# Performance work log

Measured on AMD Instinct MI355X. Metric: run time of the kernel, lower is better.

Reference implementation:

```python
import jax, jax.numpy as jnp
import numpy as np

EMBED_DIMS = [8, 16, 8]      # prod = 1024 = embed_dim
HIDDEN_DIMS = [16, 16, 16]   # prod = 4096 = hidden_dim
RANK = 16
B, S = 4, 1024


def _make_cores(key, in_dims, out_dims, rank):
    d = len(in_dims)
    ranks = [1] + [rank] * (d - 1) + [1]
    cores = []
    for k in range(d):
        key, sub = jax.random.split(key)
        shape = (ranks[k], in_dims[k], out_dims[k], ranks[k + 1])
        scale = 1.0 / np.sqrt(in_dims[k] * ranks[k])
        cores.append((scale * jax.random.normal(sub, shape, dtype=jnp.float32)))
    return cores


def setup_inputs() -> dict:
    key = jax.random.key(0)
    k_x, k1, k2, kb1, kb2 = jax.random.split(key, 5)
    x = jax.random.normal(k_x, (B, S, 1024), dtype=jnp.float32)
    fc1 = _make_cores(k1, EMBED_DIMS, HIDDEN_DIMS, RANK)
    fc2 = _make_cores(k2, HIDDEN_DIMS, EMBED_DIMS, RANK)
    b1 = 0.01 * jax.random.normal(kb1, (4096,), dtype=jnp.float32)
    b2 = 0.01 * jax.random.normal(kb2, (1024,), dtype=jnp.float32)
    return {
        "x": x,
        "fc1_c0": fc1[0], "fc1_c1": fc1[1], "fc1_c2": fc1[2], "fc1_b": b1,
        "fc2_c0": fc2[0], "fc2_c1": fc2[1], "fc2_c2": fc2[2], "fc2_b": b2,
    }


def tt_linear(x_flat, cores, bias, in_dims):
    """TT-matrix x batch-of-vectors product. x_flat: [N, prod(in_dims)].

    Cores: core_k has shape [r_{k-1}, n_k, m_k, r_k] with r_0 = r_d = 1.
    Invariant: acc is [r_{k-1}, n_k, rest] with rest laid out as
    (n_{k+1}..n_d, N, m_1..m_{k-1}).
    """
    N = x_flat.shape[0]
    acc = x_flat.reshape((N,) + tuple(in_dims))      # [N, n1..nd]
    acc = jnp.moveaxis(acc, 0, -1)                   # [n1..nd, N]
    acc = acc.reshape(in_dims[0], -1)[None]          # [1, n1, rest]
    d = len(cores)
    for k, c in enumerate(cores):
        # contract previous rank + current input mode
        acc = jnp.einsum('pnR,pnmq->Rmq', acc, c)    # [rest, m_k, r_k]
        if k < d - 1:
            n_next = in_dims[k + 1]
            R, m, q = acc.shape
            acc = acc.reshape(n_next, R // n_next, m, q)
            acc = jnp.transpose(acc, (3, 0, 1, 2)).reshape(q, n_next, -1)
    # final acc: [N * m1..m_{d-1}, m_d, 1] -> [N, M]
    return acc.reshape(N, -1) + bias


def reference(x, fc1_c0, fc1_c1, fc1_c2, fc1_b, fc2_c0, fc2_c1, fc2_c2, fc2_b):
    flat = x.reshape(-1, x.shape[-1])                        # [N, embed_dim]
    z1 = tt_linear(flat, [fc1_c0, fc1_c1, fc1_c2], fc1_b, EMBED_DIMS)   # [N, hidden]
    h1 = jax.nn.gelu(z1, approximate=False)                  # exact erf GELU (torch default)
    z2 = tt_linear(h1, [fc2_c0, fc2_c1, fc2_c2], fc2_b, HIDDEN_DIMS)    # [N, embed]
    return z2.reshape(*x.shape[:-1], z2.shape[-1])
```

## Files before the change

### kernel.cpp

```cpp
#include <hip/hip_runtime.h>
#include <stdint.h>

__device__ __forceinline__ float b2f(unsigned short u) {
    union { uint32_t i; float f; } v; v.i = ((uint32_t)u) << 16; return v.f;
}
__device__ __forceinline__ unsigned short f2b(float f) {
    union { float f; uint32_t i; } v; v.f = f;
    uint32_t r = v.i + 0x7fffu + ((v.i >> 16) & 1u);
    return (unsigned short)(r >> 16);
}

typedef __bf16 bf16x8 __attribute__((ext_vector_type(8)));
typedef float  f32x16 __attribute__((ext_vector_type(16)));

template<int N1, int N2, int N3, int M1, int M2, int M3>
__device__ __forceinline__ void build_W_fused(int blk,
                                              const float* __restrict__ c0,
                                              const float* __restrict__ c1,
                                              const float* __restrict__ c2,
                                              unsigned short* __restrict__ W,
                                              float* __restrict__ S) {
    constexpr int K = N1 * N2 * N3;
    const int n2 = blk / M2;
    const int m2 = blk % M2;

    for (int e = threadIdx.x; e < 16 * N3 * M3; e += 256) {
        const int m3 = e % M3;
        const int n3 = (e / M3) % N3;
        const int r1 = e / (M3 * N3);
        const float* c1p = c1 + ((r1 * N2 + n2) * M2 + m2) * 16;
        float s = 0.f;
#pragma unroll
        for (int r2 = 0; r2 < 16; ++r2)
            s += c1p[r2] * c2[(r2 * N3 + n3) * M3 + m3];
        S[e] = s;
    }
    __syncthreads();

    for (int e = threadIdx.x; e < N1 * M1 * M3; e += 256) {
        const int m3 = e % M3;
        const int m1 = (e / M3) % M1;
        const int n1 = e / (M3 * M1);
        const float* c0p = c0 + (n1 * M1 + m1) * 16;
        float acc[N3] = {};
#pragma unroll
        for (int r1 = 0; r1 < 16; ++r1) {
            const float c0v = c0p[r1];
#pragma unroll
            for (int n3 = 0; n3 < N3; ++n3)
                acc[n3] += c0v * S[(r1 * N3 + n3) * M3 + m3];
        }
        unsigned short ob[N3];
#pragma unroll
        for (int n3 = 0; n3 < N3; ++n3) ob[n3] = f2b(acc[n3]);
        unsigned short* dst = W + (size_t)((m1 * M2 + m2) * M3 + m3) * K
                                + (n1 * N2 + n2) * N3;
#pragma unroll
        for (int c = 0; c < N3 / 8; ++c)
            ((int4*)dst)[c] = ((const int4*)ob)[c];
    }
}

__global__ __launch_bounds__(256)
void prep_all(const float* __restrict__ c10, const float* __restrict__ c11,
              const float* __restrict__ c12,
              const float* __restrict__ c20, const float* __restrict__ c21,
              const float* __restrict__ c22,
              const float* __restrict__ x, unsigned short* __restrict__ xb,
              unsigned short* __restrict__ W1, unsigned short* __restrict__ W2) {
    __shared__ float S[16 * 128];
    const int b = blockIdx.x;
    if (b < 256) {
        build_W_fused<8, 16, 8, 16, 16, 16>(b, c10, c11, c12, W1, S);
    } else if (b < 512) {
        build_W_fused<16, 16, 16, 8, 16, 8>(b - 256, c20, c21, c22, W2, S);
    } else {
        const int t = (b - 512) * 256 + threadIdx.x;
        const float4* p = (const float4*)(x + (size_t)t * 8);
        float4 f0 = p[0], f1 = p[1];
        int4 o;
        o.x = (uint32_t)f2b(f0.x) | ((uint32_t)f2b(f0.y) << 16);
        o.y = (uint32_t)f2b(f0.z) | ((uint32_t)f2b(f0.w) << 16);
        o.z = (uint32_t)f2b(f1.x) | ((uint32_t)f2b(f1.y) << 16);
        o.w = (uint32_t)f2b(f1.z) | ((uint32_t)f2b(f1.w) << 16);
        ((int4*)xb)[t] = o;
    }
}

template<int N3, int M3>
__device__ __forceinline__ void build_T_body(int e,
                                             const float* __restrict__ c1,
                                             const float* __restrict__ c2,
                                             float* __restrict__ T) {
    int m3 = e % M3;
    int t  = e / M3;
    int n3 = t % N3;
    int rm = t / N3;
    float s = 0.f;
#pragma unroll
    for (int r2 = 0; r2 < 16; ++r2)
        s += c1[rm * 16 + r2] * c2[(r2 * N3 + n3) * M3 + m3];
    T[e] = s;
}

__global__ __launch_bounds__(256)
void prep_stage1(const float* __restrict__ c11, const float* __restrict__ c12,
                 float* __restrict__ T1,
                 const float* __restrict__ c21, const float* __restrict__ c22,
                 float* __restrict__ T2,
                 const float* __restrict__ x, unsigned short* __restrict__ xb) {
    const int b = blockIdx.x;
    if (b < 2048) {
        build_T_body<8, 16>(b * 256 + threadIdx.x, c11, c12, T1);
    } else if (b < 4096) {
        build_T_body<16, 8>((b - 2048) * 256 + threadIdx.x, c21, c22, T2);
    } else {
        const int t = (b - 4096) * 256 + threadIdx.x;
        const float4* p = (const float4*)(x + (size_t)t * 8);
        float4 f0 = p[0], f1 = p[1];
        int4 o;
        o.x = (uint32_t)f2b(f0.x) | ((uint32_t)f2b(f0.y) << 16);
        o.y = (uint32_t)f2b(f0.z) | ((uint32_t)f2b(f0.w) << 16);
        o.z = (uint32_t)f2b(f1.x) | ((uint32_t)f2b(f1.y) << 16);
        o.w = (uint32_t)f2b(f1.z) | ((uint32_t)f2b(f1.w) << 16);
        ((int4*)xb)[t] = o;
    }
}

template<int N1, int N2, int N3, int M1, int M2, int M3>
__device__ __forceinline__ void build_W_body(int t,
                                             const float* __restrict__ c0,
                                             const float* __restrict__ T,
                                             unsigned short* __restrict__ W) {
    constexpr int K = N1 * N2 * N3;
    int m3 = t % M3;
    int m2 = (t / M3) % M2;
    int n2 = (t / (M3 * M2)) % N2;
    int m1 = (t / (M3 * M2 * N2)) % M1;
    int n1 =  t / (M3 * M2 * N2 * M1);

    float c0r[16];
    const float4* c0p = (const float4*)(c0 + (n1 * M1 + m1) * 16);
#pragma unroll
    for (int i = 0; i < 4; ++i) ((float4*)c0r)[i] = c0p[i];

    float acc[N3] = {};
#pragma unroll
    for (int r1 = 0; r1 < 16; ++r1) {
        const float* Tp = T + (size_t)(((r1 * 16 + n2) * 16 + m2) * N3) * M3 + m3;
#pragma unroll
        for (int n3 = 0; n3 < N3; ++n3)
            acc[n3] += c0r[r1] * Tp[n3 * M3];
    }

    unsigned short ob[N3];
#pragma unroll
    for (int n3 = 0; n3 < N3; ++n3) ob[n3] = f2b(acc[n3]);

    unsigned short* dst = W + (size_t)((m1 * M2 + m2) * M3 + m3) * K
                            + (n1 * N2 + n2) * N3;
#pragma unroll
    for (int c = 0; c < N3 / 8; ++c)
        ((int4*)dst)[c] = ((const int4*)ob)[c];
}

template<int N1, int N2, int N3, int M1, int M2, int M3>
__global__ __launch_bounds__(256)
void build_W(const float* __restrict__ c0, const float* __restrict__ T,
             unsigned short* __restrict__ W) {
    build_W_body<N1, N2, N3, M1, M2, M3>(blockIdx.x * 256 + threadIdx.x, c0, T, W);
}

template<int BM, int BN, int KTOT, int GX, bool DO_GELU>
__global__ __launch_bounds__(512, 2)
void gemm_big(const unsigned short* __restrict__ A,
              const unsigned short* __restrict__ Bt,
              const float* __restrict__ bias,
              unsigned short* __restrict__ C,
              int Ncols)
{
    constexpr int BK   = 64;
    constexpr int NT   = KTOT / BK;
    constexpr int ASZ  = BM * BK;
    constexpr int BUFE = (BM + BN) * BK;
    constexpr int ACH  = BM / 64;
    constexpr int BCH  = BN / 64;
    constexpr int FI   = 4, FJ = 2;

    extern __shared__ unsigned short sh[];

    const int tid   = threadIdx.x;
    const int lane  = tid & 63;
    const int wave  = tid >> 6;
    const int m32   = lane & 31;
    const int khalf = lane >> 5;
    const int waveM = (wave >> 2) * 128;
    const int waveN = (wave & 3) * 64;
    const int srow  = tid >> 3;
    const int sslot = tid & 7;

    int lin = (int)blockIdx.y * GX + (int)blockIdx.x;
    const int total = GX * (int)gridDim.y;
    lin = (lin & 7) * (total >> 3) + (lin >> 3);
    const int colBase = (lin % GX) * BN;
    const int rowBase = (lin / GX) * BM;

#define BG_STAGE(B_, K0_)                                                     \
    {                                                                         \
        _Pragma("unroll")                                                     \
        for (int c = 0; c < ACH; ++c) {                                       \
            const int r  = c * 64 + srow;                                     \
            const int jg = sslot ^ (r & 7) ^ ((r >> 3) & 7);                  \
            const unsigned short* src = A +                                   \
                (size_t)(rowBase + r) * KTOT + (K0_) + jg * 8;                \
            unsigned short* dst = sh + (B_) * BUFE + c * 4096 + wave * 512;   \
            __builtin_amdgcn_global_load_lds(                                 \
                (const __attribute__((address_space(1))) void*)src,           \
                (__attribute__((address_space(3))) void*)dst, 16, 0, 0);      \
        }                                                                     \
        _Pragma("unroll")                                                     \
        for (int c = 0; c < BCH; ++c) {                                       \
            const int r  = c * 64 + srow;                                     \
            const int jg = sslot ^ (r & 7) ^ ((r >> 3) & 7);                  \
            const unsigned short* src = Bt +                                  \
                (size_t)(colBase + r) * KTOT + (K0_) + jg * 8;                \
            unsigned short* dst = sh + (B_) * BUFE + ASZ + c * 4096           \
                                  + wave * 512;                               \
            __builtin_amdgcn_global_load_lds(                                 \
                (const __attribute__((address_space(1))) void*)src,           \
                (__attribute__((address_space(3))) void*)dst, 16, 0, 0);      \
        }                                                                     \
    }

    f32x16 acc[FI][FJ] = {};

    BG_STAGE(0, 0)
    __syncthreads();

    int buf = 0;
    for (int t = 0; t < NT; ++t) {
        if (t + 1 < NT) BG_STAGE(buf ^ 1, (t + 1) * BK)

        const unsigned short* Ab = sh + buf * BUFE;
        const unsigned short* Bb = Ab + ASZ;
#pragma unroll
        for (int ks = 0; ks < 4; ++ks) {
            bf16x8 a_f[FI], b_f[FJ];
            const int g = ks * 2 + khalf;
#pragma unroll
            for (int i = 0; i < FI; ++i) {
                const int r = waveM + i * 32 + m32;
                const int key = (r & 7) ^ ((r >> 3) & 7);
                a_f[i] = *(const bf16x8*)&Ab[r * BK + ((g ^ key) << 3)];
            }
#pragma unroll
            for (int j = 0; j < FJ; ++j) {
                const int r = waveN + j * 32 + m32;
                const int key = (r & 7) ^ ((r >> 3) & 7);
                b_f[j] = *(const bf16x8*)&Bb[r * BK + ((g ^ key) << 3)];
            }
#pragma unroll
            for (int i = 0; i < FI; ++i)
#pragma unroll
                for (int j = 0; j < FJ; ++j)
                    acc[i][j] = __builtin_amdgcn_mfma_f32_32x32x16_bf16(
                        a_f[i], b_f[j], acc[i][j], 0, 0, 0);
        }
        __syncthreads();
        buf ^= 1;
    }
#undef BG_STAGE

#pragma unroll
    for (int i = 0; i < FI; ++i) {
#pragma unroll
        for (int j = 0; j < FJ; ++j) {
            const int col = colBase + waveN + j * 32 + m32;
            const float bv = bias[col];
#pragma unroll
            for (int reg = 0; reg < 16; ++reg) {
                const int row = rowBase + waveM + i * 32 +
                                (reg & 3) + 8 * (reg >> 2) + 4 * khalf;
                float z = acc[i][j][reg] + bv;
                if (DO_GELU)
                    z = 0.5f * z * (1.f + erff(z * 0.70710678118654752f));
                C[(size_t)row * Ncols + col] = f2b(z);
            }
        }
    }
}

template<int BM, int BN, int KCH, int KSTR, int GX, int GY,
         bool DO_GELU, bool ATOMIC>
__global__ __launch_bounds__(256, 4)
void gemm_sb(const unsigned short* __restrict__ A,
             const unsigned short* __restrict__ Bt,
             const float* __restrict__ bias,
             void* __restrict__ Cv,
             int Ncols)
{
    constexpr int BK  = 64;
    constexpr int NT  = KCH / BK;
    constexpr int ASZ = BM * BK;
    constexpr int ACH = BM / 32;
    constexpr int BCH = BN / 32;
    constexpr int FI  = BM / 64, FJ = BN / 64;

    extern __shared__ unsigned short sh[];

    const int tid   = threadIdx.x;
    const int lane  = tid & 63;
    const int wave  = tid >> 6;
    const int m32   = lane & 31;
    const int khalf = lane >> 5;
    const int waveM = (wave >> 1) * (BM / 2);
    const int waveN = (wave & 1) * (BN / 2);
    const int srow  = tid >> 3;
    const int sslot = tid & 7;

    int lin = ((int)blockIdx.z * GY + (int)blockIdx.y) * GX + (int)blockIdx.x;
    const int total = GX * GY * (int)gridDim.z;
    lin = (lin & 7) * (total >> 3) + (lin >> 3);
    const int colBase = (lin % GX) * BN;
    const int rowBase = ((lin / GX) % GY) * BM;
    const int kOff    = (lin / (GX * GY)) * KCH;

#define SB_STAGE(K0_)                                                         \
    {                                                                         \
        _Pragma("unroll")                                                     \
        for (int c = 0; c < ACH; ++c) {                                       \
            const int r  = c * 32 + srow;                                     \
            const int jg = sslot ^ (r & 7) ^ ((r >> 3) & 7);                  \
            const unsigned short* src = A +                                   \
                (size_t)(rowBase + r) * KSTR + (K0_) + jg * 8;                \
            unsigned short* dst = sh + c * 2048 + wave * 512;                 \
            __builtin_amdgcn_global_load_lds(                                 \
                (const __attribute__((address_space(1))) void*)src,           \
                (__attribute__((address_space(3))) void*)dst, 16, 0, 0);      \
        }                                                                     \
        _Pragma("unroll")                                                     \
        for (int c = 0; c < BCH; ++c) {                                       \
            const int r  = c * 32 + srow;                                     \
            const int jg = sslot ^ (r & 7) ^ ((r >> 3) & 7);                  \
            const unsigned short* src = Bt +                                  \
                (size_t)(colBase + r) * KSTR + (K0_) + jg * 8;                \
            unsigned short* dst = sh + ASZ + c * 2048 + wave * 512;           \
            __builtin_amdgcn_global_load_lds(                                 \
                (const __attribute__((address_space(1))) void*)src,           \
                (__attribute__((address_space(3))) void*)dst, 16, 0, 0);      \
        }                                                                     \
    }

    f32x16 acc[FI][FJ] = {};

    for (int t = 0; t < NT; ++t) {
        SB_STAGE(kOff + t * BK)
        __syncthreads();

        const unsigned short* Ab = sh;
        const unsigned short* Bb = sh + ASZ;
#pragma unroll
        for (int ks = 0; ks < 4; ++ks) {
            bf16x8 a_f[FI], b_f[FJ];
            const int g = ks * 2 + khalf;
#pragma unroll
            for (int i = 0; i < FI; ++i) {
                const int r = waveM + i * 32 + m32;
                const int key = (r & 7) ^ ((r >> 3) & 7);
                a_f[i] = *(const bf16x8*)&Ab[r * BK + ((g ^ key) << 3)];
            }
#pragma unroll
            for (int j = 0; j < FJ; ++j) {
                const int r = waveN + j * 32 + m32;
                const int key = (r & 7) ^ ((r >> 3) & 7);
                b_f[j] = *(const bf16x8*)&Bb[r * BK + ((g ^ key) << 3)];
            }
#pragma unroll
            for (int i = 0; i < FI; ++i)
#pragma unroll
                for (int j = 0; j < FJ; ++j)
                    acc[i][j] = __builtin_amdgcn_mfma_f32_32x32x16_bf16(
                        a_f[i], b_f[j], acc[i][j], 0, 0, 0);
        }
        if (t + 1 < NT) __syncthreads();
    }
#undef SB_STAGE

#pragma unroll
    for (int i = 0; i < FI; ++i) {
#pragma unroll
        for (int j = 0; j < FJ; ++j) {
            const int col = colBase + waveN + j * 32 + m32;
            const float bv = ATOMIC ? 0.f : bias[col];
#pragma unroll
            for (int reg = 0; reg < 16; ++reg) {
                const int row = rowBase + waveM + i * 32 +
                                (reg & 3) + 8 * (reg >> 2) + 4 * khalf;
                const size_t off = (size_t)row * Ncols + col;
                if (ATOMIC) {
                    unsafeAtomicAdd((float*)Cv + off, acc[i][j][reg]);
                } else {
                    float z = acc[i][j][reg] + bv;
                    if (DO_GELU) {
                        z = 0.5f * z * (1.f + erff(z * 0.70710678118654752f));
                        ((unsigned short*)Cv)[off] = f2b(z);
                    } else {
                        ((float*)Cv)[off] = z;
                    }
                }
            }
        }
    }
}

#define PC_COMPUTE(BUF)                                                       \
    {                                                                         \
        _Pragma("unroll")                                                     \
        for (int ks = 0; ks < 4; ++ks) {                                      \
            bf16x8 a_f[FI], b_f[FJ];                                          \
            _Pragma("unroll")                                                 \
            for (int i = 0; i < FI; ++i) {                                    \
                const int key = (m32 & 7) ^                                   \
                    (((waveM >> 3) + 4 * i + (m32 >> 3)) & 7);                \
                const int slot = ((ks * 2 + khalf) ^ key) * 8;                \
                a_f[i] = *(const bf16x8*)&As[(BUF) * ASZ +                    \
                          (waveM + i * 32 + m32) * BK + slot];                \
            }                                                                 \
            _Pragma("unroll")                                                 \
            for (int j = 0; j < FJ; ++j) {                                    \
                const int key = (m32 & 7) ^                                   \
                    (((waveN >> 3) + 4 * j + (m32 >> 3)) & 7);                \
                const int slot = ((ks * 2 + khalf) ^ key) * 8;                \
                b_f[j] = *(const bf16x8*)&Bs[(BUF) * BSZ +                    \
                          (waveN + j * 32 + m32) * BK + slot];                \
            }                                                                 \
            _Pragma("unroll")                                                 \
            for (int i = 0; i < FI; ++i)                                      \
                _Pragma("unroll")                                             \
                for (int j = 0; j < FJ; ++j)                                  \
                    acc[i][j] = __builtin_amdgcn_mfma_f32_32x32x16_bf16(      \
                        a_f[i], b_f[j], acc[i][j], 0, 0, 0);                  \
        }                                                                     \
    }

template<int BM, int BN, int KTOT, bool DO_GELU, bool A_F32, bool C_F32>
__global__ __launch_bounds__(512, 4)
void gemm_pc(const void* __restrict__ Av,
             const unsigned short* __restrict__ Bt,
             const float* __restrict__ bias,
             void* __restrict__ Cv,
             int Ncols) {
    constexpr int BK  = 64;
    constexpr int CA  = BM / 8;
    constexpr int CB  = BN / 8;
    constexpr int PA  = CA / 4;
    constexpr int PB  = CB / 4;
    constexpr int FI  = BM / 64;
    constexpr int FJ  = BN / 64;
    constexpr int ASZ = BM * BK;
    constexpr int BSZ = BN * BK;
    __shared__ unsigned short As[2 * ASZ];
    __shared__ unsigned short Bs[2 * BSZ];

    const int tid  = threadIdx.x;
    const int lane = tid & 63;
    const int wave = tid >> 6;
    const int rowBase = blockIdx.y * BM;
    const int colBase = blockIdx.x * BN;

    const int lr    = lane >> 3;
    const int jj    = lane & 7;
    const int m32   = lane & 31;
    const int khalf = lane >> 5;

    if (wave >= 4) {
        const int pw = wave - 4;
#pragma unroll
        for (int it = 0; it < PA; ++it) {
            const int c  = pw * PA + it;
            const int jg = jj ^ lr ^ (c & 7);
            const size_t aoff = (size_t)(rowBase + c * 8 + lr) * KTOT + jg * 8;
            int4 v;
            if (A_F32) {
                const float* ga = (const float*)Av + aoff;
                float4 f0 = *(const float4*)ga;
                float4 f1 = *(const float4*)(ga + 4);
                v.x = (uint32_t)f2b(f0.x) | ((uint32_t)f2b(f0.y) << 16);
                v.y = (uint32_t)f2b(f0.z) | ((uint32_t)f2b(f0.w) << 16);
                v.z = (uint32_t)f2b(f1.x) | ((uint32_t)f2b(f1.y) << 16);
                v.w = (uint32_t)f2b(f1.z) | ((uint32_t)f2b(f1.w) << 16);
            } else {
                v = *(const int4*)((const unsigned short*)Av + aoff);
            }
            *(int4*)&As[c * 512 + lane * 8] = v;
        }
#pragma unroll
        for (int it = 0; it < PB; ++it) {
            const int c  = pw * PB + it;
            const int jg = jj ^ lr ^ (c & 7);
            *(int4*)&Bs[c * 512 + lane * 8] =
                *(const int4*)(Bt + (size_t)(colBase + c * 8 + lr) * KTOT + jg * 8);
        }
        __syncthreads();

        int buf = 1;
        for (int k0 = BK; k0 < KTOT; k0 += BK) {
            int4 aR[PA], bR[PB];
#pragma unroll
            for (int it = 0; it < PA; ++it) {
                const int c  = pw * PA + it;
                const int jg = jj ^ lr ^ (c & 7);
                const size_t aoff = (size_t)(rowBase + c * 8 + lr) * KTOT + k0 + jg * 8;
                if (A_F32) {
                    const float* ga = (const float*)Av + aoff;
                    float4 f0 = *(const float4*)ga;
                    float4 f1 = *(const float4*)(ga + 4);
                    int4 v;
                    v.x = (uint32_t)f2b(f0.x) | ((uint32_t)f2b(f0.y) << 16);
                    v.y = (uint32_t)f2b(f0.z) | ((uint32_t)f2b(f0.w) << 16);
                    v.z = (uint32_t)f2b(f1.x) | ((uint32_t)f2b(f1.y) << 16);
                    v.w = (uint32_t)f2b(f1.z) | ((uint32_t)f2b(f1.w) << 16);
                    aR[it] = v;
                } else {
                    aR[it] = *(const int4*)((const unsigned short*)Av + aoff);
                }
            }
#pragma unroll
            for (int it = 0; it < PB; ++it) {
                const int c  = pw * PB + it;
                const int jg = jj ^ lr ^ (c & 7);
                bR[it] = *(const int4*)(Bt + (size_t)(colBase + c * 8 + lr) * KTOT + k0 + jg * 8);
            }
#pragma unroll
            for (int it = 0; it < PA; ++it) {
                const int c = pw * PA + it;
                *(int4*)&As[buf * ASZ + c * 512 + lane * 8] = aR[it];
            }
#pragma unroll
            for (int it = 0; it < PB; ++it) {
                const int c = pw * PB + it;
                *(int4*)&Bs[buf * BSZ + c * 512 + lane * 8] = bR[it];
            }
            __syncthreads();
            buf ^= 1;
        }
    } else {
        const int waveM = (wave >> 1) * (BM / 2);
        const int waveN = (wave & 1) * (BN / 2);
        f32x16 acc[FI][FJ] = {};

        __syncthreads();

        int cur = 0;
        for (int k0 = BK; k0 < KTOT; k0 += BK) {
            PC_COMPUTE(cur)
            __syncthreads();
            cur ^= 1;
        }
        PC_COMPUTE(cur)

#pragma unroll
        for (int i = 0; i < FI; ++i) {
#pragma unroll
            for (int j = 0; j < FJ; ++j) {
                const int col = colBase + waveN + j * 32 + m32;
                const float bv = bias[col];
#pragma unroll
                for (int reg = 0; reg < 16; ++reg) {
                    const int row = rowBase + waveM + i * 32 +
                                    (reg & 3) + 8 * (reg >> 2) + 4 * khalf;
                    float z = acc[i][j][reg] + bv;
                    if (DO_GELU)
                        z = 0.5f * z * (1.f + erff(z * 0.70710678118654752f));
                    const size_t off = (size_t)row * Ncols + col;
                    if (C_F32) ((float*)Cv)[off] = z;
                    else       ((unsigned short*)Cv)[off] = f2b(z);
                }
            }
        }
    }
}

extern "C" void kernel_launch(void* const* d_in, const int* in_sizes, int n_in,
                              void* d_out, int out_size, void* d_ws, size_t ws_size,
                              hipStream_t stream) {
    const float* x      = (const float*)d_in[0];
    const float* fc1_c0 = (const float*)d_in[1];
    const float* fc1_c1 = (const float*)d_in[2];
    const float* fc1_c2 = (const float*)d_in[3];
    const float* fc1_b  = (const float*)d_in[4];
    const float* fc2_c0 = (const float*)d_in[5];
    const float* fc2_c1 = (const float*)d_in[6];
    const float* fc2_c2 = (const float*)d_in[7];
    const float* fc2_b  = (const float*)d_in[8];

    char* ws = (char*)d_ws;
    const bool big = ws_size >= (48ull << 20);

    constexpr int DLDSB = 2 * (256 + 256) * 64 * 2;
    constexpr int DLDS  = 40 << 10;

    static bool attr_done = false;
    if (!attr_done) {
        attr_done = true;
        (void)hipFuncSetAttribute(
            reinterpret_cast<const void*>(&gemm_big<256, 256, 1024, 16, true>),
            hipFuncAttributeMaxDynamicSharedMemorySize, DLDSB);
    }

    if (big) {
        unsigned short* xb = (unsigned short*)d_out;
        unsigned short* W1 = (unsigned short*)ws;
        unsigned short* W2 = (unsigned short*)(ws + (8u << 20));
        unsigned short* h  = (unsigned short*)(ws + (16u << 20));

        prep_all<<<2560, 256, 0, stream>>>(fc1_c0, fc1_c1, fc1_c2,
                                           fc2_c0, fc2_c1, fc2_c2,
                                           x, xb, W1, W2);
        gemm_big<256, 256, 1024, 16, true>
            <<<dim3(16, 16), 512, DLDSB, stream>>>(xb, W1, fc1_b, h, 4096);
        gemm_sb<128, 64, 4096, 4096, 16, 32, false, false>
            <<<dim3(16, 32, 1), 256, DLDS, stream>>>(h, W2, fc2_b, d_out, 1024);
    } else {
        float* T1 = (float*)d_out;
        float* T2 = (float*)d_out + 524288;
        unsigned short* xb = (unsigned short*)((char*)d_out + (4u << 20));
        unsigned short* W = (unsigned short*)ws;
        unsigned short* h = (unsigned short*)(ws + (8u << 20));

        prep_stage1<<<6144, 256, 0, stream>>>(fc1_c1, fc1_c2, T1,
                                              fc2_c1, fc2_c2, T2, x, xb);
        build_W<8, 16, 8, 16, 16, 16><<<2048, 256, 0, stream>>>(fc1_c0, T1, W);
        gemm_pc<128, 128, 1024, true, false, false>
            <<<dim3(32, 32), 512, 0, stream>>>(xb, W, fc1_b, h, 4096);
        build_W<16, 16, 16, 8, 16, 8><<<1024, 256, 0, stream>>>(fc2_c0, T2, W);
        gemm_pc<128, 64, 4096, false, false, true>
            <<<dim3(16, 32), 512, 0, stream>>>(h, W, fc2_b, d_out, 1024);
    }
}
```

Measured before the change: 201.3 us.

## Restructure FC1 GEMM main loop to prefetch two tiles ahead with register-held fragments

The FC1 GEMM mainloop now issues two tiles of global-to-LDS loads before the loop. Each iteration reads all four k-slices of LDS fragments into registers up front, then releases the LDS buffer after half the MFMAs so the load for tile t+2 can go into the same buffer while the second half of the MFMAs runs at raised wave priority. Partial vmcnt waits replace full __syncthreads so global load latency overlaps compute instead of serializing behind it. Holding more fragments in registers raises register pressure at a 2-waves-per-SIMD launch bound, which risks spills.

Result: slower. 264.1 us (+31.2%).

```diff
diff --git a/kernel.cpp b/kernel.cpp
--- a/kernel.cpp
+++ b/kernel.cpp
@@ -173,11 +173,11 @@
 
 template<int BM, int BN, int KTOT, int GX, bool DO_GELU>
 __global__ __launch_bounds__(512, 2)
-void gemm_big(const unsigned short* __restrict__ A,
-              const unsigned short* __restrict__ Bt,
-              const float* __restrict__ bias,
-              unsigned short* __restrict__ C,
-              int Ncols)
+void gemm_rf(const unsigned short* __restrict__ A,
+             const unsigned short* __restrict__ Bt,
+             const float* __restrict__ bias,
+             unsigned short* __restrict__ C,
+             int Ncols)
 {
     constexpr int BK   = 64;
     constexpr int NT   = KTOT / BK;
@@ -205,7 +205,7 @@
     const int colBase = (lin % GX) * BN;
     const int rowBase = (lin / GX) * BM;
 
-#define BG_STAGE(B_, K0_)                                                     \
+#define RF_STAGE(B_, K0_)                                                     \
     {                                                                         \
         _Pragma("unroll")                                                     \
         for (int c = 0; c < ACH; ++c) {                                       \
@@ -234,42 +234,68 @@
 
     f32x16 acc[FI][FJ] = {};
 
-    BG_STAGE(0, 0)
-    __syncthreads();
+    RF_STAGE(0, 0)
+    RF_STAGE(1, BK)
+    asm volatile("s_waitcnt vmcnt(8)" ::: "memory");
+    __builtin_amdgcn_s_barrier();
 
     int buf = 0;
     for (int t = 0; t < NT; ++t) {
-        if (t + 1 < NT) BG_STAGE(buf ^ 1, (t + 1) * BK)
-
         const unsigned short* Ab = sh + buf * BUFE;
         const unsigned short* Bb = Ab + ASZ;
+
+        bf16x8 af[4][FI], bfr[4][FJ];
 #pragma unroll
         for (int ks = 0; ks < 4; ++ks) {
-            bf16x8 a_f[FI], b_f[FJ];
             const int g = ks * 2 + khalf;
 #pragma unroll
             for (int i = 0; i < FI; ++i) {
                 const int r = waveM + i * 32 + m32;
                 const int key = (r & 7) ^ ((r >> 3) & 7);
-                a_f[i] = *(const bf16x8*)&Ab[r * BK + ((g ^ key) << 3)];
+                af[ks][i] = *(const bf16x8*)&Ab[r * BK + ((g ^ key) << 3)];
             }
 #pragma unroll
             for (int j = 0; j < FJ; ++j) {
                 const int r = waveN + j * 32 + m32;
                 const int key = (r & 7) ^ ((r >> 3) & 7);
-                b_f[j] = *(const bf16x8*)&Bb[r * BK + ((g ^ key) << 3)];
-            }
+                bfr[ks][j] = *(const bf16x8*)&Bb[r * BK + ((g ^ key) << 3)];
+            }
+        }
+
+#pragma unroll
+        for (int ks = 0; ks < 2; ++ks)
 #pragma unroll
             for (int i = 0; i < FI; ++i)
 #pragma unroll
                 for (int j = 0; j < FJ; ++j)
                     acc[i][j] = __builtin_amdgcn_mfma_f32_32x32x16_bf16(
-                        a_f[i], b_f[j], acc[i][j], 0, 0, 0);
-        }
+                        af[ks][i], bfr[ks][j], acc[i][j], 0, 0, 0);
+
         __syncthreads();
+
+        if (t + 2 < NT) RF_STAGE(buf, (t + 2) * BK)
+
+        __builtin_amdgcn_s_setprio(1);
+#pragma unroll
+        for (int ks = 2; ks < 4; ++ks)
+#pragma unroll
+            for (int i = 0; i < FI; ++i)
+#pragma unroll
+                for (int j = 0; j < FJ; ++j)
+                    acc[i][j] = __builtin_amdgcn_mfma_f32_32x32x16_bf16(
+                        af[ks][i], bfr[ks][j], acc[i][j], 0, 0, 0);
+        __builtin_amdgcn_s_setprio(0);
+
+        if (t + 2 < NT) {
+            asm volatile("s_waitcnt vmcnt(8)" ::: "memory");
+            __builtin_amdgcn_s_barrier();
+        } else if (t + 1 < NT) {
+            asm volatile("s_waitcnt vmcnt(0)" ::: "memory");
+            __builtin_amdgcn_s_barrier();
+        }
         buf ^= 1;
     }
-#undef BG_STAGE
+#undef RF_STAGE
 
 #pragma unroll
     for (int i = 0; i < FI; ++i) {
@@ -597,15 +623,15 @@
     char* ws = (char*)d_ws;
     const bool big = ws_size >= (48ull << 20);
 
-    constexpr int DLDSB = 2 * (256 + 256) * 64 * 2;
+    constexpr int DLDSR = 2 * (256 + 256) * 64 * 2;
     constexpr int DLDS  = 40 << 10;
 
     static bool attr_done = false;
     if (!attr_done) {
         attr_done = true;
         (void)hipFuncSetAttribute(
-            reinterpret_cast<const void*>(&gemm_big<256, 256, 1024, 16, true>),
-            hipFuncAttributeMaxDynamicSharedMemorySize, DLDSB);
+            reinterpret_cast<const void*>(&gemm_rf<256, 256, 1024, 16, true>),
+            hipFuncAttributeMaxDynamicSharedMemorySize, DLDSR);
     }
 
     if (big) {
@@ -617,8 +643,8 @@
         prep_all<<<2560, 256, 0, stream>>>(fc1_c0, fc1_c1, fc1_c2,
                                            fc2_c0, fc2_c1, fc2_c2,
                                            x, xb, W1, W2);
-        gemm_big<256, 256, 1024, 16, true>
-            <<<dim3(16, 16), 512, DLDSB, stream>>>(xb, W1, fc1_b, h, 4096);
+        gemm_rf<256, 256, 1024, 16, true>
+            <<<dim3(16, 16), 512, DLDSR, stream>>>(xb, W1, fc1_b, h, 4096);
         gemm_sb<128, 64, 4096, 4096, 16, 32, false, false>
             <<<dim3(16, 32, 1), 256, DLDS, stream>>>(h, W2, fc2_b, d_out, 1024);
     } else {
```

## Enlarge second-GEMM tiles with split-K atomics over a bias-prefilled output

Applied to the files above, without the earlier changes.

The second projection GEMM now uses 256x128 block tiles, with each wave computing a 128x64 sub-tile, and splits K into two halves across blockIdx.z. Partial sums are accumulated with float atomics into the output. A new bias_fill kernel pre-initialises that output with the broadcast bias. The aim is more data reuse per block, since larger tiles mean fewer global/LDS loads per FLOP, while keeping enough blocks to cover the CUs. The cost is one extra launch, doubled atomic write traffic to the output, higher register pressure (launch bounds lowered to 3), and only 256 blocks in the grid.

Result: slower. 274.5 us (+36.3%).

```diff
diff --git a/kernel.cpp b/kernel.cpp
--- a/kernel.cpp
+++ b/kernel.cpp
@@ -85,6 +85,12 @@
         o.w = (uint32_t)f2b(f1.z) | ((uint32_t)f2b(f1.w) << 16);
         ((int4*)xb)[t] = o;
     }
+}
+
+__global__ __launch_bounds__(256)
+void bias_fill(const float* __restrict__ b, float4* __restrict__ out) {
+    int t = blockIdx.x * 256 + threadIdx.x;
+    out[t] = ((const float4*)b)[t & 255];
 }
 
 template<int N3, int M3>
@@ -290,21 +296,19 @@
     }
 }
 
-template<int BM, int BN, int KCH, int KSTR, int GX, int GY,
-         bool DO_GELU, bool ATOMIC>
-__global__ __launch_bounds__(256, 4)
-void gemm_sb(const unsigned short* __restrict__ A,
-             const unsigned short* __restrict__ Bt,
-             const float* __restrict__ bias,
-             void* __restrict__ Cv,
-             int Ncols)
+template<int BM, int BN, int KCH, int KSTR, int GX, int GY>
+__global__ __launch_bounds__(256, 3)
+void gemm_sb2(const unsigned short* __restrict__ A,
+              const unsigned short* __restrict__ Bt,
+              float* __restrict__ Cv,
+              int Ncols)
 {
     constexpr int BK  = 64;
     constexpr int NT  = KCH / BK;
     constexpr int ASZ = BM * BK;
     constexpr int ACH = BM / 32;
     constexpr int BCH = BN / 32;
-    constexpr int FI  = BM / 64, FJ = BN / 64;
+    constexpr int FI  = 4, FJ = 2;
 
     extern __shared__ unsigned short sh[];
 
@@ -313,8 +317,8 @@
     const int wave  = tid >> 6;
     const int m32   = lane & 31;
     const int khalf = lane >> 5;
-    const int waveM = (wave >> 1) * (BM / 2);
-    const int waveN = (wave & 1) * (BN / 2);
+    const int waveM = (wave >> 1) * 128;
+    const int waveN = (wave & 1) * 64;
     const int srow  = tid >> 3;
     const int sslot = tid & 7;
 
@@ -325,7 +329,7 @@
     const int rowBase = ((lin / GX) % GY) * BM;
     const int kOff    = (lin / (GX * GY)) * KCH;
 
-#define SB_STAGE(K0_)                                                         \
+#define S2_STAGE(K0_)                                                         \
     {                                                                         \
         _Pragma("unroll")                                                     \
         for (int c = 0; c < ACH; ++c) {                                       \
@@ -354,7 +358,7 @@
     f32x16 acc[FI][FJ] = {};
 
     for (int t = 0; t < NT; ++t) {
-        SB_STAGE(kOff + t * BK)
+        S2_STAGE(kOff + t * BK)
         __syncthreads();
 
         const unsigned short* Ab = sh;
@@ -384,30 +388,19 @@
         }
         if (t + 1 < NT) __syncthreads();
     }
-#undef SB_STAGE
+#undef S2_STAGE
 
 #pragma unroll
     for (int i = 0; i < FI; ++i) {
 #pragma unroll
         for (int j = 0; j < FJ; ++j) {
             const int col = colBase + waveN + j * 32 + m32;
-            const float bv = ATOMIC ? 0.f : bias[col];
 #pragma unroll
             for (int reg = 0; reg < 16; ++reg) {
                 const int row = rowBase + waveM + i * 32 +
                                 (reg & 3) + 8 * (reg >> 2) + 4 * khalf;
-                const size_t off = (size_t)row * Ncols + col;
-                if (ATOMIC) {
-                    unsafeAtomicAdd((float*)Cv + off, acc[i][j][reg]);
-                } else {
-                    float z = acc[i][j][reg] + bv;
-                    if (DO_GELU) {
-                        z = 0.5f * z * (1.f + erff(z * 0.70710678118654752f));
-                        ((unsigned short*)Cv)[off] = f2b(z);
-                    } else {
-                        ((float*)Cv)[off] = z;
-                    }
-                }
+                unsafeAtomicAdd(Cv + (size_t)row * Ncols + col,
+                                acc[i][j][reg]);
             }
         }
     }
@@ -598,7 +591,7 @@
     const bool big = ws_size >= (48ull << 20);
 
     constexpr int DLDSB = 2 * (256 + 256) * 64 * 2;
-    constexpr int DLDS  = 40 << 10;
+    constexpr int DLDS2 = (256 + 128) * 64 * 2;
 
     static bool attr_done = false;
     if (!attr_done) {
@@ -619,8 +612,9 @@
                                            x, xb, W1, W2);
         gemm_big<256, 256, 1024, 16, true>
             <<<dim3(16, 16), 512, DLDSB, stream>>>(xb, W1, fc1_b, h, 4096);
-        gemm_sb<128, 64, 4096, 4096, 16, 32, false, false>
-            <<<dim3(16, 32, 1), 256, DLDS, stream>>>(h, W2, fc2_b, d_out, 1024);
+        bias_fill<<<4096, 256, 0, stream>>>(fc2_b, (float4*)d_out);
+        gemm_sb2<256, 128, 2048, 4096, 8, 16>
+            <<<dim3(8, 16, 2), 256, DLDS2, stream>>>(h, W2, (float*)d_out, 1024);
     } else {
         float* T1 = (float*)d_out;
         float* T2 = (float*)d_out + 524288;
```
